# Kernel optimization log

Hardware: AMD Instinct MI355X
Metric: run time of the kernel (lower is better)

Reference implementation:

```python
import jax, jax.numpy as jnp
import numpy as np

B, N, M, C, H = 8, 2048, 1024, 512, 8
D = C // H  # per-head dim = 64


def setup_inputs() -> dict:
    key = jax.random.key(0)
    ks = jax.random.split(key, 4)
    x = jax.random.normal(ks[0], (B, N, C), dtype=jnp.float32)
    global_tokens = jax.random.normal(ks[1], (B, M, C), dtype=jnp.float32)
    Wq = jax.random.normal(ks[2], (C, C), dtype=jnp.float32) * 0.02
    bq = jnp.zeros((C,), dtype=jnp.float32)
    Wkv = jax.random.normal(ks[3], (C, 2 * C), dtype=jnp.float32) * 0.02
    bkv = jnp.zeros((2 * C,), dtype=jnp.float32)
    return {"x": x, "global_tokens": global_tokens, "Wq": Wq, "bq": bq,
            "Wkv": Wkv, "bkv": bkv}


def reference(x, global_tokens, Wq, bq, Wkv, bkv):
    # q from x, k/v from global_tokens (LinearProjection with query=True)
    q = (x @ Wq + bq).reshape(B, N, H, D).transpose(0, 2, 1, 3)        # [B,H,N,D]
    kv = (global_tokens @ Wkv + bkv).reshape(B, M, 2, H, D)
    k = kv[:, :, 0].transpose(0, 2, 1, 3)                              # [B,H,M,D]
    v = kv[:, :, 1].transpose(0, 2, 1, 3)                              # [B,H,M,D]
    # NOTE: original module applies no 1/sqrt(D) scaling in forward
    attn = jnp.einsum('bhnd,bhmd->bhnm', q, k)                         # [B,H,N,M]
    attn = jax.nn.softmax(attn, axis=-1)
    out = jnp.einsum('bhnm,bhmd->bhnd', attn, v)                       # [B,H,N,D]
    return out.transpose(0, 2, 1, 3).reshape(B, N, C)
```

## Files before the change

### kernel.cpp

```cpp
#include <hip/hip_runtime.h>
#include <hip/hip_bf16.h>


typedef __bf16 bf16_t;
typedef __bf16 bf16x8 __attribute__((ext_vector_type(8)));
typedef __bf16 bf16x4 __attribute__((ext_vector_type(4)));
typedef float floatx16 __attribute__((ext_vector_type(16)));
typedef unsigned int uintx4 __attribute__((ext_vector_type(4)));
typedef unsigned int uintx2 __attribute__((ext_vector_type(2)));

#define KDIM 512
#define QSCALE 1.44269504088896f

#define WAITVM(N) asm volatile("s_waitcnt vmcnt(" #N ")" ::: "memory")
#define BAR()                                  \
  do {                                         \
    __builtin_amdgcn_s_barrier();              \
    asm volatile("" ::: "memory");             \
  } while (0)

__device__ __forceinline__ unsigned pack2(float a, float b) {
  unsigned short ua = __builtin_bit_cast(unsigned short, (bf16_t)a);
  unsigned short ub = __builtin_bit_cast(unsigned short, (bf16_t)b);
  return (unsigned)ua | ((unsigned)ub << 16);
}

__device__ __forceinline__ float fexp2(float x) {
#if __has_builtin(__builtin_amdgcn_exp2f)
  return __builtin_amdgcn_exp2f(x);
#else
  return __exp2f(x);
#endif
}

__device__ __forceinline__ bf16x8 cvt8(const float4 a, const float4 b) {
  bf16x8 r;
  r[0] = (bf16_t)a.x; r[1] = (bf16_t)a.y; r[2] = (bf16_t)a.z; r[3] = (bf16_t)a.w;
  r[4] = (bf16_t)b.x; r[5] = (bf16_t)b.y; r[6] = (bf16_t)b.z; r[7] = (bf16_t)b.w;
  return r;
}

__device__ __forceinline__ void gl_lds16(const bf16_t* g, bf16_t* l) {
#if __has_builtin(__builtin_amdgcn_global_load_lds)
  __builtin_amdgcn_global_load_lds(
      (const __attribute__((address_space(1))) unsigned int*)(g),
      (__attribute__((address_space(3))) unsigned int*)(l), 16, 0, 0);
#else
  *(bf16x8*)l = *(const bf16x8*)g;
#endif
}

__global__ __launch_bounds__(256) void prep_kernel(
    const float* __restrict__ Wq, const float* __restrict__ Wkv,
    const float* __restrict__ x, const float* __restrict__ gt,
    bf16_t* __restrict__ Wqt, bf16_t* __restrict__ Wkvt,
    bf16_t* __restrict__ Aq, bf16_t* __restrict__ Akv) {
  __shared__ float tile[64][65];
  const int blk = blockIdx.x;
  const int t = threadIdx.x;
  if (blk < 192) {
    const float* in; bf16_t* out; int N, bx, by;
    if (blk < 64) { in = Wq; out = Wqt; N = 512; bx = blk & 7; by = blk >> 3; }
    else { int t2 = blk - 64; in = Wkv; out = Wkvt; N = 1024; bx = t2 & 15; by = t2 >> 4; }
    const int c0 = bx * 64, k0 = by * 64;
#pragma unroll
    for (int i = 0; i < 16; ++i) {
      int idx = t + i * 256;
      int kk = idx >> 6, cc = idx & 63;
      tile[kk][cc] = in[(size_t)(k0 + kk) * N + (c0 + cc)];
    }
    __syncthreads();
#pragma unroll
    for (int j = 0; j < 2; ++j) {
      int unit = t + j * 256;
      int cc = unit >> 3, ks = (unit & 7) * 8;
      int c = c0 + cc, k = k0 + ks;
      bf16x8 v;
#pragma unroll
      for (int i = 0; i < 8; ++i) v[i] = (bf16_t)tile[ks + i][cc];
      const int k5 = k & 31;
      const int chunk = ((c & 127) >> 5) * 2 + (k5 >> 4);
      *(bf16x8*)(&out[(size_t)((c >> 7) * 16 + (k >> 5)) * 4096 + chunk * 512 +
                      (c & 31) * 8 + ((k5 >> 3) & 1) * 256]) = v;
    }
  } else {
    int idx = blk - 192;
    const float* src; bf16_t* dst; int rt, kt2;
    if (idx < 2048) { src = x; dst = Aq; rt = idx >> 4; kt2 = idx & 15; }
    else { int i2 = idx - 2048; src = gt; dst = Akv; rt = i2 >> 4; kt2 = i2 & 15; }
    const int row = rt * 128 + (t >> 1);
    const int kb = kt2 * 32 + (t & 1) * 16;
    const float* p = src + (size_t)row * KDIM + kb;
    float4 f0 = *(const float4*)(p);
    float4 f1 = *(const float4*)(p + 4);
    float4 f2 = *(const float4*)(p + 8);
    float4 f3 = *(const float4*)(p + 12);
    bf16x8 o0 = cvt8(f0, f1), o1 = cvt8(f2, f3);
    const int chunk = ((row & 127) >> 5) * 2 + (t & 1);
    bf16_t* ob = dst + (size_t)(rt * 16 + kt2) * 4096 + chunk * 512 + (row & 31) * 8;
    *(bf16x8*)(ob) = o0;
    *(bf16x8*)(ob + 256) = o1;
  }
}

__global__ __launch_bounds__(256) void proj_gemm_kernel(
    const bf16_t* __restrict__ Aq, const bf16_t* __restrict__ Akv,
    const bf16_t* __restrict__ Wqt, const bf16_t* __restrict__ Wkvt,
    const float* __restrict__ bq, const float* __restrict__ bkv,
    bf16_t* __restrict__ Qf, bf16_t* __restrict__ Kf, bf16_t* __restrict__ Vf) {
  __shared__ bf16_t lds[3][8192];
  const int blk = blockIdx.x;
  int mode, bx, by;
  const bf16_t* Ab; const bf16_t* Wb; const float* bias;
  if (blk < 512) { mode = 0; bx = blk & 3; by = blk >> 2; Ab = Aq; Wb = Wqt; bias = bq; }
  else { int tt = blk - 512; mode = 1; bx = tt & 7; by = tt >> 3; Ab = Akv; Wb = Wkvt; bias = bkv; }

  const int tid = threadIdx.x;
  const int wave = tid >> 6, L = tid & 63;
  const int l5 = L & 31, hf = L >> 5;
  const int wr = wave >> 1, wc = wave & 1;
  const int rb = by * 128, cb = bx * 128;

  const bf16_t* Abase = Ab + (size_t)by * 16 * 4096 + L * 8;
  const bf16_t* Wbase = Wb + (size_t)bx * 16 * 4096 + L * 8;

  auto dma = [&](int buf, int kt) {
#pragma unroll
    for (int j = 0; j < 4; ++j) {
      const int s = wave * 4 + j;
      const bf16_t* g = (s < 8) ? (Abase + (size_t)kt * 4096 + s * 512)
                                : (Wbase + (size_t)kt * 4096 + (s - 8) * 512);
      gl_lds16(g, &lds[buf][(s < 8 ? s * 512 : 4096 + (s - 8) * 512) + L * 8]);
    }
  };

  floatx16 acc[2][2] = {};

  auto kstep = [&](int cur) {
    bf16x8 af[2][2], wf[2][2];
#pragma unroll
    for (int rs = 0; rs < 2; ++rs)
#pragma unroll
      for (int kh = 0; kh < 2; ++kh)
        af[rs][kh] = *(const bf16x8*)(&lds[cur][((wr * 2 + rs) * 2 + kh) * 512 + L * 8]);
#pragma unroll
    for (int cs = 0; cs < 2; ++cs)
#pragma unroll
      for (int kh = 0; kh < 2; ++kh)
        wf[cs][kh] = *(const bf16x8*)(&lds[cur][4096 + ((wc * 2 + cs) * 2 + kh) * 512 + L * 8]);
    __builtin_amdgcn_s_setprio(1);
#pragma unroll
    for (int rs = 0; rs < 2; ++rs)
#pragma unroll
      for (int cs = 0; cs < 2; ++cs)
#pragma unroll
        for (int kh = 0; kh < 2; ++kh)
          acc[rs][cs] = __builtin_amdgcn_mfma_f32_32x32x16_bf16(
              af[rs][kh], wf[cs][kh], acc[rs][cs], 0, 0, 0);
    __builtin_amdgcn_s_setprio(0);
  };

  dma(0, 0);
  dma(1, 1);

  int cur = 0, pf = 2;
  for (int kt = 0; kt < 15; ++kt) {
    WAITVM(4);
    BAR();
    if (kt <= 13) {
      dma(pf, kt + 2);
      pf = (pf == 2) ? 0 : pf + 1;
    }
    kstep(cur);
    cur = (cur == 2) ? 0 : cur + 1;
  }
  WAITVM(0);
  BAR();
  kstep(cur);

#pragma unroll
  for (int rs = 0; rs < 2; ++rs)
#pragma unroll
    for (int cs = 0; cs < 2; ++cs) {
      const int col = cb + wc * 64 + cs * 32 + l5;
      const float bv = bias[col];
      const int grb = rb + wr * 64 + rs * 32;
      if (mode == 0) {
        const int hh = col >> 6, d = col & 63;
        const int dof = (d >> 3) * 256 + (d & 7);
#pragma unroll
        for (int r = 0; r < 16; ++r) {
          int gr = grb + (r & 3) + 8 * (r >> 2) + 4 * hf;
          int b = gr >> 11, n = gr & 2047;
          Qf[(size_t)(b * 8 + hh) * 131072 + (n >> 5) * 2048 + dof + (n & 31) * 8] =
              (bf16_t)((acc[rs][cs][r] + bv) * QSCALE);
        }
      } else if (col < 512) {
        const int hh = col >> 6, d = col & 63;
        const int dof = (d >> 3) * 256 + (d & 7);
#pragma unroll
        for (int r = 0; r < 16; ++r) {
          int gr = grb + (r & 3) + 8 * (r >> 2) + 4 * hf;
          int b = gr >> 10, m = gr & 1023;
          Kf[(size_t)(b * 8 + hh) * 65536 + (m >> 5) * 2048 + dof + (m & 31) * 8] =
              (bf16_t)(acc[rs][cs][r] + bv);
        }
      } else {
        const int cc = col - 512;
        const int hh = cc >> 6, d = cc & 63;
        const int dof = (d >> 5) * 1024 + (d & 31) * 8;
#pragma unroll
        for (int rq = 0; rq < 4; ++rq) {
          int gr = grb + 8 * rq + 4 * hf;
          int b = gr >> 10, m = gr & 1023;
          bf16x4 pk;
          pk[0] = (bf16_t)(acc[rs][cs][rq * 4 + 0] + bv);
          pk[1] = (bf16_t)(acc[rs][cs][rq * 4 + 1] + bv);
          pk[2] = (bf16_t)(acc[rs][cs][rq * 4 + 2] + bv);
          pk[3] = (bf16_t)(acc[rs][cs][rq * 4 + 3] + bv);
          *(bf16x4*)(&Vf[(size_t)(b * 8 + hh) * 65536 + (m >> 5) * 2048 + dof +
                         ((m >> 4) & 1) * 512 + ((m >> 3) & 1) * 256 + (m & 7)]) = pk;
        }
      }
    }
}

__global__ __launch_bounds__(256, 4) void flash_attn_kernel(
    const bf16_t* __restrict__ Qf, const bf16_t* __restrict__ Kf,
    const bf16_t* __restrict__ Vf, float* __restrict__ out) {
  __shared__ bf16_t kv[4][4096];
  const int tid = threadIdx.x;
  const int wave = tid >> 6, L = tid & 63;
  const int l5 = L & 31, hf = L >> 5;
  const int bh = blockIdx.y;
  const int b = bh >> 3, hh = bh & 7;
  const int nb = blockIdx.x * 128 + wave * 32;

  const bf16_t* Qp = Qf + (size_t)bh * 131072 + (nb >> 5) * 2048 + L * 8;
  const bf16_t* Kb = Kf + (size_t)bh * 65536 + L * 8;
  const bf16_t* Vb = Vf + (size_t)bh * 65536 + L * 8;

  bf16x8 qf[4];
#pragma unroll
  for (int kc = 0; kc < 4; ++kc) qf[kc] = *(const bf16x8*)(Qp + kc * 512);

  bf16x8 ones;
#pragma unroll
  for (int i = 0; i < 8; ++i) ones[i] = (bf16_t)1.0f;

  floatx16 o0 = {}, o1 = {}, lacc = {};

  auto dma = [&](int buf, int s) {
#pragma unroll
    for (int j = 0; j < 2; ++j) {
      const int q = wave * 2 + j;
      const bf16_t* g = (q < 4) ? (Kb + (size_t)s * 2048 + q * 512)
                                : (Vb + (size_t)s * 2048 + (q - 4) * 512);
      gl_lds16(g, &kv[buf][(q < 4 ? q * 512 : 2048 + (q - 4) * 512) + L * 8]);
    }
  };

  auto subtile = [&](int s) {
    const bf16_t* kb = &kv[s & 3][L * 8];
    const bf16_t* vb = &kv[s & 3][2048 + L * 8];
    bf16x8 kf4[4];
#pragma unroll
    for (int kc = 0; kc < 4; ++kc) kf4[kc] = *(const bf16x8*)(kb + kc * 512);
    floatx16 sa = {};
    __builtin_amdgcn_s_setprio(1);
#pragma unroll
    for (int kc = 0; kc < 4; ++kc)
      sa = __builtin_amdgcn_mfma_f32_32x32x16_bf16(kf4[kc], qf[kc], sa, 0, 0, 0);
    __builtin_amdgcn_s_setprio(0);
    bf16x8 vf4[4];
#pragma unroll
    for (int j = 0; j < 4; ++j) vf4[j] = *(const bf16x8*)(vb + j * 512);
    unsigned w[8];
#pragma unroll
    for (int i = 0; i < 8; ++i) {
      float pa = fexp2(sa[2 * i]), pb = fexp2(sa[2 * i + 1]);
      w[i] = pack2(pa, pb);
    }
    uintx4 fw0, fw1;
#if __has_builtin(__builtin_amdgcn_permlane32_swap)
    {
      uintx2 r0 = __builtin_amdgcn_permlane32_swap(w[0], w[2], false, false);
      uintx2 r1 = __builtin_amdgcn_permlane32_swap(w[1], w[3], false, false);
      uintx2 r2 = __builtin_amdgcn_permlane32_swap(w[4], w[6], false, false);
      uintx2 r3 = __builtin_amdgcn_permlane32_swap(w[5], w[7], false, false);
      fw0.x = r0[0]; fw0.z = r0[1];
      fw0.y = r1[0]; fw0.w = r1[1];
      fw1.x = r2[0]; fw1.z = r2[1];
      fw1.y = r3[0]; fw1.w = r3[1];
    }
#else
    {
      unsigned sw[8];
#pragma unroll
      for (int i = 0; i < 8; ++i) sw[i] = __shfl_xor(w[i], 32);
      fw0.x = hf ? sw[2] : w[0]; fw0.y = hf ? sw[3] : w[1];
      fw0.z = hf ? w[2] : sw[0]; fw0.w = hf ? w[3] : sw[1];
      fw1.x = hf ? sw[6] : w[4]; fw1.y = hf ? sw[7] : w[5];
      fw1.z = hf ? w[6] : sw[4]; fw1.w = hf ? w[7] : sw[5];
    }
#endif
    bf16x8 pf0 = __builtin_bit_cast(bf16x8, fw0);
    bf16x8 pf1 = __builtin_bit_cast(bf16x8, fw1);
    __builtin_amdgcn_s_setprio(1);
    lacc = __builtin_amdgcn_mfma_f32_32x32x16_bf16(ones, pf0, lacc, 0, 0, 0);
    lacc = __builtin_amdgcn_mfma_f32_32x32x16_bf16(ones, pf1, lacc, 0, 0, 0);
    o0 = __builtin_amdgcn_mfma_f32_32x32x16_bf16(vf4[0], pf0, o0, 0, 0, 0);
    o0 = __builtin_amdgcn_mfma_f32_32x32x16_bf16(vf4[1], pf1, o0, 0, 0, 0);
    o1 = __builtin_amdgcn_mfma_f32_32x32x16_bf16(vf4[2], pf0, o1, 0, 0, 0);
    o1 = __builtin_amdgcn_mfma_f32_32x32x16_bf16(vf4[3], pf1, o1, 0, 0, 0);
    __builtin_amdgcn_s_setprio(0);
  };

  dma(0, 0);
  dma(1, 1);
  dma(2, 2);

  for (int s = 0; s < 30; ++s) {
    WAITVM(4);
    BAR();
    if (s <= 28) dma((s + 3) & 3, s + 3);
    subtile(s);
  }
  WAITVM(2);
  BAR();
  subtile(30);
  WAITVM(0);
  BAR();
  subtile(31);

  __syncthreads();

  const float inv = 1.0f / lacc[0];

  float* lob = (float*)(&kv[0][0]) + wave * (32 * 36);
  const size_t orow = (size_t)b * 2048 + nb;
#pragma unroll
  for (int pass = 0; pass < 2; ++pass) {
    const floatx16& oo = pass ? o1 : o0;
#pragma unroll
    for (int i = 0; i < 8; ++i) {
      const int d = 2 * (i & 1) + 8 * (i >> 1) + 4 * hf;
      float2 a;
      a.x = oo[2 * i] * inv; a.y = oo[2 * i + 1] * inv;
      *(float2*)(&lob[l5 * 36 + d]) = a;
    }
#pragma unroll
    for (int j = 0; j < 4; ++j) {
      int chunk = j * 64 + L;
      int n = chunk >> 3, c = chunk & 7;
      float4 v = *(const float4*)(&lob[n * 36 + c * 4]);
      *(float4*)(&out[(orow + n) * 512 + hh * 64 + pass * 32 + c * 4]) = v;
    }
  }
}

extern "C" void kernel_launch(void* const* d_in, const int* in_sizes, int n_in,
                              void* d_out, int out_size, void* d_ws, size_t ws_size,
                              hipStream_t stream) {
  (void)in_sizes; (void)n_in; (void)out_size; (void)ws_size;
  const float* x   = (const float*)d_in[0];
  const float* gt  = (const float*)d_in[1];
  const float* Wq  = (const float*)d_in[2];
  const float* bq  = (const float*)d_in[3];
  const float* Wkv = (const float*)d_in[4];
  const float* bkv = (const float*)d_in[5];
  float* out = (float*)d_out;

  bf16_t* Wqt  = (bf16_t*)d_ws;
  bf16_t* Wkvt = Wqt + (size_t)512 * 512;
  bf16_t* Qf   = Wkvt + (size_t)1024 * 512;
  bf16_t* Kf   = Qf + (size_t)64 * 2048 * 64;
  bf16_t* Vf   = Kf + (size_t)64 * 1024 * 64;
  bf16_t* Aq   = (bf16_t*)d_out;
  bf16_t* Akv  = Aq + (size_t)16384 * 512;

  prep_kernel<<<3264, 256, 0, stream>>>(Wq, Wkv, x, gt, Wqt, Wkvt, Aq, Akv);
  proj_gemm_kernel<<<1024, 256, 0, stream>>>(Aq, Akv, Wqt, Wkvt, bq, bkv, Qf, Kf, Vf);
  flash_attn_kernel<<<dim3(16, 64), 256, 0, stream>>>(Qf, Kf, Vf, out);
}
```

Measured before the change: 180.7 us.

## Fuse fp32-to-bf16 activation conversion into projection GEMM A-tile loads

Activation conversion and tiling move out of the prep kernel and into the projection GEMM. The GEMM now loads fp32 x/global_tokens rows into registers, converts them to bf16 and writes them to LDS, while weights still use direct global-to-LDS copies. This drops the separate bf16 round trip for activations through global memory. The change also switches from a triple-buffered to a double-buffered pipeline with syncthreads, and remaps block indices so that blocks sharing weight tiles are interleaved. In exchange, each GEMM block reads twice as many activation bytes, and the register staging may expose more load latency.

```diff
diff --git a/kernel.cpp b/kernel.cpp
--- a/kernel.cpp
+++ b/kernel.cpp
@@ -52,68 +52,48 @@
 
 __global__ __launch_bounds__(256) void prep_kernel(
     const float* __restrict__ Wq, const float* __restrict__ Wkv,
-    const float* __restrict__ x, const float* __restrict__ gt,
-    bf16_t* __restrict__ Wqt, bf16_t* __restrict__ Wkvt,
-    bf16_t* __restrict__ Aq, bf16_t* __restrict__ Akv) {
+    bf16_t* __restrict__ Wqt, bf16_t* __restrict__ Wkvt) {
   __shared__ float tile[64][65];
   const int blk = blockIdx.x;
   const int t = threadIdx.x;
-  if (blk < 192) {
-    const float* in; bf16_t* out; int N, bx, by;
-    if (blk < 64) { in = Wq; out = Wqt; N = 512; bx = blk & 7; by = blk >> 3; }
-    else { int t2 = blk - 64; in = Wkv; out = Wkvt; N = 1024; bx = t2 & 15; by = t2 >> 4; }
-    const int c0 = bx * 64, k0 = by * 64;
-#pragma unroll
-    for (int i = 0; i < 16; ++i) {
-      int idx = t + i * 256;
-      int kk = idx >> 6, cc = idx & 63;
-      tile[kk][cc] = in[(size_t)(k0 + kk) * N + (c0 + cc)];
-    }
-    __syncthreads();
-#pragma unroll
-    for (int j = 0; j < 2; ++j) {
-      int unit = t + j * 256;
-      int cc = unit >> 3, ks = (unit & 7) * 8;
-      int c = c0 + cc, k = k0 + ks;
-      bf16x8 v;
-#pragma unroll
-      for (int i = 0; i < 8; ++i) v[i] = (bf16_t)tile[ks + i][cc];
-      const int k5 = k & 31;
-      const int chunk = ((c & 127) >> 5) * 2 + (k5 >> 4);
-      *(bf16x8*)(&out[(size_t)((c >> 7) * 16 + (k >> 5)) * 4096 + chunk * 512 +
-                      (c & 31) * 8 + ((k5 >> 3) & 1) * 256]) = v;
-    }
-  } else {
-    int idx = blk - 192;
-    const float* src; bf16_t* dst; int rt, kt2;
-    if (idx < 2048) { src = x; dst = Aq; rt = idx >> 4; kt2 = idx & 15; }
-    else { int i2 = idx - 2048; src = gt; dst = Akv; rt = i2 >> 4; kt2 = i2 & 15; }
-    const int row = rt * 128 + (t >> 1);
-    const int kb = kt2 * 32 + (t & 1) * 16;
-    const float* p = src + (size_t)row * KDIM + kb;
-    float4 f0 = *(const float4*)(p);
-    float4 f1 = *(const float4*)(p + 4);
-    float4 f2 = *(const float4*)(p + 8);
-    float4 f3 = *(const float4*)(p + 12);
-    bf16x8 o0 = cvt8(f0, f1), o1 = cvt8(f2, f3);
-    const int chunk = ((row & 127) >> 5) * 2 + (t & 1);
-    bf16_t* ob = dst + (size_t)(rt * 16 + kt2) * 4096 + chunk * 512 + (row & 31) * 8;
-    *(bf16x8*)(ob) = o0;
-    *(bf16x8*)(ob + 256) = o1;
+  const float* in; bf16_t* out; int N, bx, by;
+  if (blk < 64) { in = Wq; out = Wqt; N = 512; bx = blk & 7; by = blk >> 3; }
+  else { int t2 = blk - 64; in = Wkv; out = Wkvt; N = 1024; bx = t2 & 15; by = t2 >> 4; }
+  const int c0 = bx * 64, k0 = by * 64;
+#pragma unroll
+  for (int i = 0; i < 16; ++i) {
+    int idx = t + i * 256;
+    int kk = idx >> 6, cc = idx & 63;
+    tile[kk][cc] = in[(size_t)(k0 + kk) * N + (c0 + cc)];
+  }
+  __syncthreads();
+#pragma unroll
+  for (int j = 0; j < 2; ++j) {
+    int unit = t + j * 256;
+    int cc = unit >> 3, ks = (unit & 7) * 8;
+    int c = c0 + cc, k = k0 + ks;
+    bf16x8 v;
+#pragma unroll
+    for (int i = 0; i < 8; ++i) v[i] = (bf16_t)tile[ks + i][cc];
+    const int k5 = k & 31;
+    const int chunk = ((c & 127) >> 5) * 2 + (k5 >> 4);
+    *(bf16x8*)(&out[(size_t)((c >> 7) * 16 + (k >> 5)) * 4096 + chunk * 512 +
+                    (c & 31) * 8 + ((k5 >> 3) & 1) * 256]) = v;
   }
 }
 
 __global__ __launch_bounds__(256) void proj_gemm_kernel(
-    const bf16_t* __restrict__ Aq, const bf16_t* __restrict__ Akv,
+    const float* __restrict__ x, const float* __restrict__ gt,
     const bf16_t* __restrict__ Wqt, const bf16_t* __restrict__ Wkvt,
     const float* __restrict__ bq, const float* __restrict__ bkv,
     bf16_t* __restrict__ Qf, bf16_t* __restrict__ Kf, bf16_t* __restrict__ Vf) {
-  __shared__ bf16_t lds[3][8192];
-  const int blk = blockIdx.x;
+  __shared__ bf16_t lds[2][8192];
+  const int raw = blockIdx.x;
+  const int blk = (raw & 7) * 128 + (raw >> 3);
   int mode, bx, by;
-  const bf16_t* Ab; const bf16_t* Wb; const float* bias;
-  if (blk < 512) { mode = 0; bx = blk & 3; by = blk >> 2; Ab = Aq; Wb = Wqt; bias = bq; }
-  else { int tt = blk - 512; mode = 1; bx = tt & 7; by = tt >> 3; Ab = Akv; Wb = Wkvt; bias = bkv; }
+  const float* Asrc; const bf16_t* Wb; const float* bias;
+  if (blk < 512) { mode = 0; bx = blk & 3; by = blk >> 2; Asrc = x; Wb = Wqt; bias = bq; }
+  else { int tt = blk - 512; mode = 1; bx = tt & 7; by = tt >> 3; Asrc = gt; Wb = Wkvt; bias = bkv; }
 
   const int tid = threadIdx.x;
   const int wave = tid >> 6, L = tid & 63;
@@ -121,22 +101,47 @@
   const int wr = wave >> 1, wc = wave & 1;
   const int rb = by * 128, cb = bx * 128;
 
-  const bf16_t* Abase = Ab + (size_t)by * 16 * 4096 + L * 8;
+  const int arow = tid >> 1;
+  const int akoct = tid & 1;
+  const float* asrc = Asrc + (size_t)(rb + arow) * KDIM + akoct * 16;
+  const int aoff = (((arow & 127) >> 5) * 2 + akoct) * 512 + (arow & 31) * 8;
+
   const bf16_t* Wbase = Wb + (size_t)bx * 16 * 4096 + L * 8;
 
-  auto dma = [&](int buf, int kt) {
-#pragma unroll
-    for (int j = 0; j < 4; ++j) {
-      const int s = wave * 4 + j;
-      const bf16_t* g = (s < 8) ? (Abase + (size_t)kt * 4096 + s * 512)
-                                : (Wbase + (size_t)kt * 4096 + (s - 8) * 512);
-      gl_lds16(g, &lds[buf][(s < 8 ? s * 512 : 4096 + (s - 8) * 512) + L * 8]);
-    }
-  };
+  auto dmaW = [&](int buf, int kt) {
+#pragma unroll
+    for (int j = 0; j < 2; ++j) {
+      const int s = wave * 2 + j;
+      gl_lds16(Wbase + (size_t)kt * 4096 + s * 512, &lds[buf][4096 + s * 512 + L * 8]);
+    }
+  };
+
+  float4 a0, a1, a2, a3;
+  auto loadA = [&](int kt) {
+    const float* p = asrc + kt * 32;
+    a0 = *(const float4*)(p);
+    a1 = *(const float4*)(p + 4);
+    a2 = *(const float4*)(p + 8);
+    a3 = *(const float4*)(p + 12);
+  };
+  auto writeA = [&](int buf) {
+    bf16_t* d = &lds[buf][aoff];
+    *(bf16x8*)(d) = cvt8(a0, a1);
+    *(bf16x8*)(d + 256) = cvt8(a2, a3);
+  };
+
+  loadA(0);
+  dmaW(0, 0);
+  writeA(0);
+  __syncthreads();
 
   floatx16 acc[2][2] = {};
-
-  auto kstep = [&](int cur) {
+  for (int kt = 0; kt < 16; ++kt) {
+    const int cur = kt & 1;
+    if (kt < 15) {
+      loadA(kt + 1);
+      dmaW(cur ^ 1, kt + 1);
+    }
     bf16x8 af[2][2], wf[2][2];
 #pragma unroll
     for (int rs = 0; rs < 2; ++rs)
@@ -158,25 +163,9 @@
           acc[rs][cs] = __builtin_amdgcn_mfma_f32_32x32x16_bf16(
               af[rs][kh], wf[cs][kh], acc[rs][cs], 0, 0, 0);
     __builtin_amdgcn_s_setprio(0);
-  };
-
-  dma(0, 0);
-  dma(1, 1);
-
-  int cur = 0, pf = 2;
-  for (int kt = 0; kt < 15; ++kt) {
-    WAITVM(4);
-    BAR();
-    if (kt <= 13) {
-      dma(pf, kt + 2);
-      pf = (pf == 2) ? 0 : pf + 1;
-    }
-    kstep(cur);
-    cur = (cur == 2) ? 0 : cur + 1;
-  }
-  WAITVM(0);
-  BAR();
-  kstep(cur);
+    if (kt < 15) writeA(cur ^ 1);
+    __syncthreads();
+  }
 
 #pragma unroll
   for (int rs = 0; rs < 2; ++rs)
@@ -376,10 +365,8 @@
   bf16_t* Qf   = Wkvt + (size_t)1024 * 512;
   bf16_t* Kf   = Qf + (size_t)64 * 2048 * 64;
   bf16_t* Vf   = Kf + (size_t)64 * 1024 * 64;
-  bf16_t* Aq   = (bf16_t*)d_out;
-  bf16_t* Akv  = Aq + (size_t)16384 * 512;
-
-  prep_kernel<<<3264, 256, 0, stream>>>(Wq, Wkv, x, gt, Wqt, Wkvt, Aq, Akv);
-  proj_gemm_kernel<<<1024, 256, 0, stream>>>(Aq, Akv, Wqt, Wkvt, bq, bkv, Qf, Kf, Vf);
+
+  prep_kernel<<<192, 256, 0, stream>>>(Wq, Wkv, Wqt, Wkvt);
+  proj_gemm_kernel<<<1024, 256, 0, stream>>>(x, gt, Wqt, Wkvt, bq, bkv, Qf, Kf, Vf);
   flash_attn_kernel<<<dim3(16, 64), 256, 0, stream>>>(Qf, Kf, Vf, out);
 }
```

Result: slower. 193.0 us (+6.8%).

## Stage Q/K epilogue through swizzled LDS, double-buffer K loop, remap block order

Applied to the files above, without the earlier changes.

The projection GEMM epilogue for Q and K now writes each wave's tile into a swizzled LDS staging area and then emits coalesced 16-byte global stores, replacing scattered 2-byte stores. The K loop moves from a triple-buffered, vmcnt-tracked prefetch to a simpler double buffer with a full __syncthreads per step, which halves LDS use but leaves less load latency hidden. Block indices are also permuted so that consecutive launched blocks interleave Q and KV tiles.

```diff
diff --git a/kernel.cpp b/kernel.cpp
--- a/kernel.cpp
+++ b/kernel.cpp
@@ -108,8 +108,9 @@
     const bf16_t* __restrict__ Wqt, const bf16_t* __restrict__ Wkvt,
     const float* __restrict__ bq, const float* __restrict__ bkv,
     bf16_t* __restrict__ Qf, bf16_t* __restrict__ Kf, bf16_t* __restrict__ Vf) {
-  __shared__ bf16_t lds[3][8192];
-  const int blk = blockIdx.x;
+  __shared__ bf16_t lds[2][8192];
+  const int raw = blockIdx.x;
+  const int blk = (raw & 7) * 128 + (raw >> 3);
   int mode, bx, by;
   const bf16_t* Ab; const bf16_t* Wb; const float* bias;
   if (blk < 512) { mode = 0; bx = blk & 3; by = blk >> 2; Ab = Aq; Wb = Wqt; bias = bq; }
@@ -134,9 +135,13 @@
     }
   };
 
+  dma(0, 0);
+  __syncthreads();
+
   floatx16 acc[2][2] = {};
-
-  auto kstep = [&](int cur) {
+  for (int kt = 0; kt < 16; ++kt) {
+    const int cur = kt & 1;
+    if (kt < 15) dma(cur ^ 1, kt + 1);
     bf16x8 af[2][2], wf[2][2];
 #pragma unroll
     for (int rs = 0; rs < 2; ++rs)
@@ -158,54 +163,56 @@
           acc[rs][cs] = __builtin_amdgcn_mfma_f32_32x32x16_bf16(
               af[rs][kh], wf[cs][kh], acc[rs][cs], 0, 0, 0);
     __builtin_amdgcn_s_setprio(0);
-  };
-
-  dma(0, 0);
-  dma(1, 1);
-
-  int cur = 0, pf = 2;
-  for (int kt = 0; kt < 15; ++kt) {
-    WAITVM(4);
-    BAR();
-    if (kt <= 13) {
-      dma(pf, kt + 2);
-      pf = (pf == 2) ? 0 : pf + 1;
-    }
-    kstep(cur);
-    cur = (cur == 2) ? 0 : cur + 1;
-  }
-  WAITVM(0);
-  BAR();
-  kstep(cur);
-
-#pragma unroll
-  for (int rs = 0; rs < 2; ++rs)
-#pragma unroll
-    for (int cs = 0; cs < 2; ++cs) {
-      const int col = cb + wc * 64 + cs * 32 + l5;
-      const float bv = bias[col];
-      const int grb = rb + wr * 64 + rs * 32;
-      if (mode == 0) {
-        const int hh = col >> 6, d = col & 63;
-        const int dof = (d >> 3) * 256 + (d & 7);
+    __syncthreads();
+  }
+
+  const int colb = cb + wc * 64;
+  char* stc = (char*)(&lds[0][0] + wave * 4096);
+  const int gr0 = rb + wr * 64;
+
+  if (mode == 0 || colb < 512) {
+    bf16_t* dstT; size_t base2;
+    const int hh = (colb & 511) >> 6;
+    if (mode == 0) {
+      const int b = gr0 >> 11, n0 = gr0 & 2047;
+      base2 = 2 * ((size_t)(b * 8 + hh) * 131072 + (size_t)(n0 >> 5) * 2048);
+      dstT = Qf;
+    } else {
+      const int b = gr0 >> 10, m0 = gr0 & 1023;
+      base2 = 2 * ((size_t)(b * 8 + hh) * 65536 + (size_t)(m0 >> 5) * 2048);
+      dstT = Kf;
+    }
+#pragma unroll
+    for (int rs = 0; rs < 2; ++rs)
+#pragma unroll
+      for (int cs = 0; cs < 2; ++cs) {
+        const int d = cs * 32 + l5;
+        const float bv = bias[colb + cs * 32 + l5];
 #pragma unroll
         for (int r = 0; r < 16; ++r) {
-          int gr = grb + (r & 3) + 8 * (r >> 2) + 4 * hf;
-          int b = gr >> 11, n = gr & 2047;
-          Qf[(size_t)(b * 8 + hh) * 131072 + (n >> 5) * 2048 + dof + (n & 31) * 8] =
-              (bf16_t)((acc[rs][cs][r] + bv) * QSCALE);
+          const int nl = rs * 32 + (r & 3) + 8 * (r >> 2) + 4 * hf;
+          float v = acc[rs][cs][r] + bv;
+          if (mode == 0) v *= QSCALE;
+          int q = ((nl >> 5) << 12) | ((d >> 3) << 9) | ((nl & 31) << 4) | ((d & 7) << 1);
+          q ^= ((q >> 9) & 7) << 4;
+          *(bf16_t*)(stc + q) = (bf16_t)v;
         }
-      } else if (col < 512) {
-        const int hh = col >> 6, d = col & 63;
-        const int dof = (d >> 3) * 256 + (d & 7);
-#pragma unroll
-        for (int r = 0; r < 16; ++r) {
-          int gr = grb + (r & 3) + 8 * (r >> 2) + 4 * hf;
-          int b = gr >> 10, m = gr & 1023;
-          Kf[(size_t)(b * 8 + hh) * 65536 + (m >> 5) * 2048 + dof + (m & 31) * 8] =
-              (bf16_t)(acc[rs][cs][r] + bv);
-        }
-      } else {
+      }
+#pragma unroll
+    for (int g = 0; g < 8; ++g) {
+      const int q = g * 1024 + L * 16;
+      const int qs = q ^ (((q >> 9) & 7) << 4);
+      bf16x8 vv = *(const bf16x8*)(stc + qs);
+      *(bf16x8*)((char*)dstT + base2 + q) = vv;
+    }
+  } else {
+#pragma unroll
+    for (int rs = 0; rs < 2; ++rs)
+#pragma unroll
+      for (int cs = 0; cs < 2; ++cs) {
+        const int col = colb + cs * 32 + l5;
+        const float bv = bias[col];
+        const int grb = gr0 + rs * 32;
         const int cc = col - 512;
         const int hh = cc >> 6, d = cc & 63;
         const int dof = (d >> 5) * 1024 + (d & 31) * 8;
@@ -222,7 +229,7 @@
                          ((m >> 4) & 1) * 512 + ((m >> 3) & 1) * 256 + (m & 7)]) = pk;
         }
       }
-    }
+  }
 }
 
 __global__ __launch_bounds__(256, 4) void flash_attn_kernel(
```

After: 174.8 us. -3.3%, faster.
